# Kernel optimization log

Measured on AMD Instinct MI355X. Metric: run time of the kernel, lower is better.

## Reference

```python
import jax, jax.numpy as jnp
import numpy as np

B, C_IN, H, W = 4, 2048, 64, 64
C_INTER = C_IN // 4          # 512
C_QK = C_INTER // 8          # 64
C_OUT = 512


def conv3x3(x, w):
    # x: [B,C,H,W], w: [O,I,3,3], padding=1, no bias
    return jax.lax.conv_general_dilated(
        x, w, window_strides=(1, 1), padding=((1, 1), (1, 1)),
        dimension_numbers=('NCHW', 'OIHW', 'NCHW'))


def criss_cross_attention(x, qw, kw, vw, gamma):
    # x: [B,Ci,H,W]; qw,kw: [Cqk,Ci]; vw: [Ci,Ci]; gamma: scalar
    b, c, h, w = x.shape
    q = jnp.einsum('bchw,oc->bohw', x, qw)
    k = jnp.einsum('bchw,oc->bohw', x, kw)
    v = jnp.einsum('bchw,oc->bohw', x, vw)
    # column (H-axis) affinity with -inf diagonal to avoid double self-count
    eH = jnp.einsum('bchw,bciw->bhwi', q, k)                  # [B,H,W,H]
    diag = jnp.eye(h, dtype=bool)[None, :, None, :]           # [1,H,1,H]
    eH = jnp.where(diag, -jnp.inf, eH)
    # row (W-axis) affinity
    eW = jnp.einsum('bchw,bchj->bhwj', q, k)                  # [B,H,W,W]
    att = jax.nn.softmax(jnp.concatenate([eH, eW], axis=-1), axis=-1)
    attH, attW = att[..., :h], att[..., h:]
    outH = jnp.einsum('bhwi,bciw->bchw', attH, v)
    outW = jnp.einsum('bhwj,bchj->bchw', attW, v)
    return gamma * (outH + outW) + x


def setup_inputs() -> dict:
    key = jax.random.key(0)
    ks = jax.random.split(key, 8)
    s = 0.02
    return {
        'x': jax.random.normal(ks[0], (B, C_IN, H, W), jnp.float32),
        'conva_w': jax.random.normal(ks[1], (C_INTER, C_IN, 3, 3), jnp.float32) * s,
        'q_w': jax.random.normal(ks[2], (C_QK, C_INTER), jnp.float32) * s,
        'k_w': jax.random.normal(ks[3], (C_QK, C_INTER), jnp.float32) * s,
        'v_w': jax.random.normal(ks[4], (C_INTER, C_INTER), jnp.float32) * s,
        'gamma': jax.random.normal(ks[5], (), jnp.float32) * 0.1,
        'convb_w': jax.random.normal(ks[6], (C_INTER, C_INTER, 3, 3), jnp.float32) * s,
        'bottleneck_w': jax.random.normal(ks[7], (C_OUT, C_IN + C_INTER, 3, 3), jnp.float32) * s,
        'recurrence': 2,
    }


def reference(x, conva_w, q_w, k_w, v_w, gamma, convb_w, bottleneck_w, recurrence):
    out = conv3x3(x, conva_w)
    for _ in range(recurrence):
        out = criss_cross_attention(out, q_w, k_w, v_w, gamma)
    out = conv3x3(out, convb_w)
    out = conv3x3(jnp.concatenate([x, out], axis=1), bottleneck_w)
    return out
```

## Files before the change

### kernel.cpp

```cpp
#include <hip/hip_runtime.h>
#include <hip/hip_bf16.h>
#include <stdint.h>

typedef unsigned short u16;
typedef __bf16 bf16x8 __attribute__((ext_vector_type(8)));
typedef float f32x4 __attribute__((ext_vector_type(4)));

#define DEVINL __device__ __forceinline__

DEVINL float bf2f(u16 v) {
    union { uint32_t u; float f; } c; c.u = ((uint32_t)v) << 16; return c.f;
}
DEVINL u16 f2bf(float f) {
    union { float f; uint32_t u; } c; c.f = f;
    uint32_t x = c.u;
    x += 0x7fffu + ((x >> 16) & 1u);
    return (u16)(x >> 16);
}

DEVINL void load_lds16(const u16* g, char* lds_uniform_base) {
    __builtin_amdgcn_global_load_lds(
        (const __attribute__((address_space(1))) void*)g,
        (__attribute__((address_space(3))) void*)lds_uniform_base,
        16, 0, 0);
}

template<int OM>
__launch_bounds__(256)
__global__ void conv_gemm(const u16* __restrict__ in, int IH, int IW, int inC, int cofs,
                          int K, int ntaps, const u16* __restrict__ wt, int N,
                          void* __restrict__ outp, int outC, int nwg)
{
    __shared__ __align__(16) u16 ldsA[2][8192];
    __shared__ __align__(16) u16 ldsB[2][8192];

    const int id  = blockIdx.x;
    const int swz = (id & 7) * (nwg >> 3) + (id >> 3);
    const int m0 = (swz & 127) << 7;
    const int n0 = (swz >> 7) << 7;

    const int tid  = threadIdx.x;
    const int lane = tid & 63;
    const int wv   = tid >> 6;
    const int l7 = lane & 7, l3 = lane >> 3;
    const int g  = lane >> 4;
    const int cOff = (l7 ^ l3) << 3;

    const int wn = (wv & 1) * 64;
    const int wm = (wv >> 1) * 64;

    f32x4 acc[4][4];
#pragma unroll
    for (int i = 0; i < 4; ++i)
#pragma unroll
        for (int j = 0; j < 4; ++j) acc[i][j] = (f32x4){0.f, 0.f, 0.f, 0.f};

    const u16* aBase = wt + (size_t)(n0 + wv * 32 + l3) * K + cOff;
    const u16* bBase[4];
#pragma unroll
    for (int q = 0; q < 4; ++q) {
        int mA = m0 + wv * 32 + q * 8 + l3;
        int bb = mA >> 12, yy = (mA >> 6) & 63, xx = mA & 63;
        bBase[q] = in + ((size_t)(bb * IH + yy) * IW + xx) * inC + cofs + cOff;
    }

    const int kpt = K >> 6;
    const int nsteps = ntaps * kpt;
    int s_tap = 0, s_k0 = 0;
    size_t s_wofs = 0;
    int s_xofs = 0;

    auto STAGE = [&](int buf) {
        char* la = (char*)ldsA[buf] + wv * 4096;
        char* lb = (char*)ldsB[buf] + wv * 4096;
        const u16* wp = aBase + s_wofs;
        const int xo = s_xofs;
#pragma unroll
        for (int q = 0; q < 4; ++q) {
            load_lds16(wp + (size_t)(q * 8) * K, la + q * 1024);
            load_lds16(bBase[q] + xo,            lb + q * 1024);
        }
    };
    auto ADV = [&]() {
        ++s_tap;
        if (s_tap == ntaps) { s_tap = 0; s_k0 += 64; }
        int ty = s_tap / 3, tx = s_tap % 3;
        s_wofs = (size_t)s_tap * N * K + s_k0;
        s_xofs = (ty * IW + tx) * inC + s_k0;
    };

    STAGE(0); ADV();
    int cur = 0;
    const int rb = (lane & 15) << 7;

    for (int s = 0; s < nsteps; ++s) {
        __syncthreads();
        if (s + 1 < nsteps) { STAGE(cur ^ 1); ADV(); }

        const char* laW = (const char*)ldsA[cur] + (wn << 7);
        const char* lbW = (const char*)ldsB[cur] + (wm << 7);
#pragma unroll
        for (int kk = 0; kk < 2; ++kk) {
            const int ca = (((kk << 2) + g) ^ l7) << 4;
            bf16x8 af[4], bfr[4];
#pragma unroll
            for (int f = 0; f < 4; ++f) {
                af[f]  = *(const bf16x8*)(laW + (f << 11) + rb + ca);
                bfr[f] = *(const bf16x8*)(lbW + (f << 11) + rb + ca);
            }
#pragma unroll
            for (int fn = 0; fn < 4; ++fn)
#pragma unroll
                for (int fm = 0; fm < 4; ++fm)
                    acc[fn][fm] = __builtin_amdgcn_mfma_f32_16x16x32_bf16(
                        af[fn], bfr[fm], acc[fn][fm], 0, 0, 0);
        }
        cur ^= 1;
    }

    const int rn = (lane >> 4) * 4;
    const int cm = lane & 15;
#pragma unroll
    for (int fn = 0; fn < 4; ++fn) {
#pragma unroll
        for (int fm = 0; fm < 4; ++fm) {
            const int n = n0 + wn + fn * 16 + rn;
            const int m = m0 + wm + fm * 16 + cm;
            const int b = m >> 12, y = (m >> 6) & 63, x = m & 63;
            f32x4 v = acc[fn][fm];
            if constexpr (OM == 1) {
                ushort4 pk;
                pk.x = f2bf(v[0]); pk.y = f2bf(v[1]); pk.z = f2bf(v[2]); pk.w = f2bf(v[3]);
                *(ushort4*)((u16*)outp + (size_t)m * outC + n) = pk;
            } else if constexpr (OM == 2) {
                ushort4 pk;
                pk.x = f2bf(v[0]); pk.y = f2bf(v[1]); pk.z = f2bf(v[2]); pk.w = f2bf(v[3]);
                size_t o = ((size_t)(b * 66 + y + 1) * 66 + (x + 1)) * 2560 + 2048 + n;
                *(ushort4*)((u16*)outp + o) = pk;
            } else {
                float* op = (float*)outp;
#pragma unroll
                for (int r = 0; r < 4; ++r)
                    op[((size_t)(b * 512 + n + r) << 12) + (y << 6) + x] = v[r];
            }
        }
    }
}


__global__ void wtrans(const float* __restrict__ w, u16* __restrict__ wo, int O, int C)
{
    int idx = blockIdx.x * 256 + threadIdx.x;
    int total = O * C;
    if (idx >= total) return;
    const float* src = w + (size_t)idx * 9;
    float v[9];
#pragma unroll
    for (int t = 0; t < 9; ++t) v[t] = src[t];
#pragma unroll
    for (int t = 0; t < 9; ++t) wo[(size_t)t * total + idx] = f2bf(v[t]);
}

__global__ void wqkv_concat(const float* __restrict__ q, const float* __restrict__ k,
                            const float* __restrict__ v, u16* __restrict__ o)
{
    int idx = blockIdx.x * 256 + threadIdx.x;
    if (idx >= 640 * 512) return;
    int row = idx >> 9;
    float val = (row < 64) ? q[idx] : (row < 128) ? k[idx - 64 * 512] : v[idx - 128 * 512];
    o[idx] = f2bf(val);
}

__global__ void nchw_to_nhwc_pad(const float* __restrict__ x, u16* __restrict__ xp)
{
    size_t idx = (size_t)blockIdx.x * 256 + threadIdx.x;
    int m  = (int)(idx & 16383);
    int cc = (int)(idx >> 14);
    int xw = m & 63, y = (m >> 6) & 63, b = m >> 12;
    const float* xs = x + ((size_t)(b * 2048 + cc * 8)) * 4096 + (y << 6) + xw;
    union { u16 u[8]; uint4 v4; } tmp;
#pragma unroll
    for (int j = 0; j < 8; ++j) tmp.u[j] = f2bf(xs[(size_t)j * 4096]);
    u16* dst = xp + ((size_t)(b * 66 + y + 1) * 66 + (xw + 1)) * 2560 + cc * 8;
    *(uint4*)dst = tmp.v4;
}

__global__ void pad512(const u16* __restrict__ F, u16* __restrict__ FP)
{
    size_t idx = (size_t)blockIdx.x * 256 + threadIdx.x;
    int cc = (int)(idx & 63);
    int m  = (int)(idx >> 6);
    int xw = m & 63, y = (m >> 6) & 63, b = m >> 12;
    const uint4* src = (const uint4*)(F + (size_t)m * 512 + cc * 8);
    uint4* dst = (uint4*)(FP + ((size_t)(b * 66 + y + 1) * 66 + (xw + 1)) * 512 + cc * 8);
    *dst = *src;
}

__global__ void zero_border(u16* __restrict__ P, int C)
{
    int idx = blockIdx.x * 256 + threadIdx.x;
    int cw = C >> 3;
    int total = 4 * 260 * cw;
    if (idx >= total) return;
    int ch   = (idx % cw) * 8;
    int cell = (idx / cw) % 260;
    int b    = idx / (cw * 260);
    int y, x;
    if (cell < 66)       { y = 0;              x = cell;       }
    else if (cell < 132) { y = 65;             x = cell - 66;  }
    else if (cell < 196) { y = cell - 132 + 1; x = 0;          }
    else                 { y = cell - 196 + 1; x = 65;         }
    size_t o = ((size_t)(b * 66 + y) * 66 + x) * C + ch;
    *(uint4*)(P + o) = (uint4){0, 0, 0, 0};
}

__global__ void fill7777(float* __restrict__ o, int n)
{
    int idx = blockIdx.x * 256 + threadIdx.x;
    if (idx < n) o[idx] = 7777.0f;
}

#define NEGBIG -1.0e30f

__global__ void att_score(const u16* __restrict__ QKV, float* __restrict__ ATT)
{
    const int bid0 = blockIdx.x;
    const bool isW = bid0 >= 512;
    const int bid = bid0 & 511;
    const int half = bid >> 8;
    const int b = (bid >> 6) & 3, rc = bid & 63;
    __shared__ float q[32][65], kk[64][65];
    const int tid = threadIdx.x;
    for (int p = tid; p < 2048; p += 256) {
        int r = p >> 6, c = p & 63;
        int row = half * 32 + r;
        size_t m = isW ? (size_t)((b << 12) + (rc << 6) + row)
                       : (size_t)((b << 12) + (row << 6) + rc);
        q[r][c] = bf2f(QKV[m * 640 + c]);
    }
    for (int p = tid; p < 4096; p += 256) {
        int r = p >> 6, c = p & 63;
        size_t m = isW ? (size_t)((b << 12) + (rc << 6) + r)
                       : (size_t)((b << 12) + (r << 6) + rc);
        kk[r][c] = bf2f(QKV[m * 640 + 64 + c]);
    }
    __syncthreads();
    for (int p = tid; p < 2048; p += 256) {
        int r = p >> 6, i = p & 63;
        float s = 0.f;
#pragma unroll 8
        for (int c = 0; c < 64; ++c) s += q[r][c] * kk[i][c];
        int row = half * 32 + r;
        if (!isW) {
            if (i == row) s = NEGBIG;
            ATT[(size_t)((b << 12) + (row << 6) + rc) * 128 + i] = s;
        } else {
            ATT[(size_t)((b << 12) + (rc << 6) + row) * 128 + 64 + i] = s;
        }
    }
}

DEVINL void softmax32(float (*A)[132], int tid)
{
    const int row = tid >> 3, sub = tid & 7;
    float lm = -3.4e38f;
#pragma unroll
    for (int i = sub * 16; i < sub * 16 + 16; ++i) lm = fmaxf(lm, A[row][i]);
    lm = fmaxf(lm, __shfl_xor(lm, 1));
    lm = fmaxf(lm, __shfl_xor(lm, 2));
    lm = fmaxf(lm, __shfl_xor(lm, 4));
    float ls = 0.f;
#pragma unroll
    for (int i = sub * 16; i < sub * 16 + 16; ++i) {
        float e = __expf(A[row][i] - lm);
        A[row][i] = e;
        ls += e;
    }
    ls += __shfl_xor(ls, 1);
    ls += __shfl_xor(ls, 2);
    ls += __shfl_xor(ls, 4);
    float inv = 1.f / ls;
#pragma unroll
    for (int i = sub * 16; i < sub * 16 + 16; ++i) A[row][i] *= inv;
}

__launch_bounds__(256)
__global__ void att_outH(const u16* __restrict__ QKV, const float* __restrict__ ATT,
                         float* __restrict__ OH)
{
    const int bid = blockIdx.x;
    const int half = bid >> 8;
    const int b = (bid >> 6) & 3, x = bid & 63;
    __shared__ float A[32][132];
    const int tid = threadIdx.x;
    for (int p = tid; p < 1024; p += 256) {
        int r = p >> 5, q4 = p & 31;
        *(f32x4*)&A[r][q4 * 4] = *(const f32x4*)
            &ATT[(size_t)((b << 12) + ((half * 32 + r) << 6) + x) * 128 + q4 * 4];
    }
    __syncthreads();
    softmax32(A, tid);
    __syncthreads();
    const int wv = tid >> 6, lane = tid & 63;
    const int r0 = wv * 8;
    float acc[8][8];
#pragma unroll
    for (int cc = 0; cc < 8; ++cc)
#pragma unroll
        for (int yy = 0; yy < 8; ++yy) acc[cc][yy] = 0.f;
    for (int i = 0; i < 64; ++i) {
        float a[8];
#pragma unroll
        for (int yy = 0; yy < 8; ++yy) a[yy] = A[r0 + yy][i];
        const u16* vrow = QKV + (size_t)((b << 12) + (i << 6) + x) * 640 + 128;
#pragma unroll
        for (int cc = 0; cc < 8; ++cc) {
            float v = bf2f(vrow[cc * 64 + lane]);
#pragma unroll
            for (int yy = 0; yy < 8; ++yy) acc[cc][yy] += a[yy] * v;
        }
    }
    const int y0 = half * 32 + r0;
#pragma unroll
    for (int cc = 0; cc < 8; ++cc)
#pragma unroll
        for (int yy = 0; yy < 8; ++yy)
            OH[(size_t)((b << 12) + ((y0 + yy) << 6) + x) * 512 + cc * 64 + lane]
                = acc[cc][yy];
}

__launch_bounds__(256)
__global__ void att_outW_combine(const u16* __restrict__ QKV, const float* __restrict__ ATT,
                                 const float* __restrict__ OH, const u16* __restrict__ Fin,
                                 u16* __restrict__ Fout, const float* __restrict__ gamma)
{
    const int bid = blockIdx.x;
    const int half = bid >> 8;
    const int b = (bid >> 6) & 3, y = bid & 63;
    const size_t mb = (size_t)((b << 12) + (y << 6));
    __shared__ float A[32][132];
    const int tid = threadIdx.x;
    for (int p = tid; p < 1024; p += 256) {
        int r = p >> 5, q4 = p & 31;
        *(f32x4*)&A[r][q4 * 4] = *(const f32x4*)
            &ATT[(mb + half * 32 + r) * 128 + q4 * 4];
    }
    const float g = gamma[0];
    __syncthreads();
    softmax32(A, tid);
    __syncthreads();
    const int wv = tid >> 6, lane = tid & 63;
    const int r0 = wv * 8;
    float acc[8][8];
#pragma unroll
    for (int cc = 0; cc < 8; ++cc)
#pragma unroll
        for (int xx = 0; xx < 8; ++xx) acc[cc][xx] = 0.f;
    for (int j = 0; j < 64; ++j) {
        float a[8];
#pragma unroll
        for (int xx = 0; xx < 8; ++xx) a[xx] = A[r0 + xx][64 + j];
        const u16* vrow = QKV + (mb + j) * 640 + 128;
#pragma unroll
        for (int cc = 0; cc < 8; ++cc) {
            float v = bf2f(vrow[cc * 64 + lane]);
#pragma unroll
            for (int xx = 0; xx < 8; ++xx) acc[cc][xx] += a[xx] * v;
        }
    }
    const int x0 = half * 32 + r0;
#pragma unroll
    for (int cc = 0; cc < 8; ++cc) {
#pragma unroll
        for (int xx = 0; xx < 8; ++xx) {
            size_t m = mb + x0 + xx;
            size_t o = m * 512 + cc * 64 + lane;
            Fout[o] = f2bf(g * (OH[o] + acc[cc][xx]) + bf2f(Fin[o]));
        }
    }
}

static constexpr size_t ALN = 512;
static inline size_t alup(size_t v) { return (v + ALN - 1) & ~(ALN - 1); }

extern "C" void kernel_launch(void* const* d_in, const int* in_sizes, int n_in,
                              void* d_out, int out_size, void* d_ws, size_t ws_size,
                              hipStream_t stream)
{
    (void)in_sizes; (void)n_in;
    const float* x       = (const float*)d_in[0];
    const float* conva_w = (const float*)d_in[1];
    const float* q_w     = (const float*)d_in[2];
    const float* k_w     = (const float*)d_in[3];
    const float* v_w     = (const float*)d_in[4];
    const float* gamma   = (const float*)d_in[5];
    const float* convb_w = (const float*)d_in[6];
    const float* bneck_w = (const float*)d_in[7];

    const size_t XP_B   = (size_t)4 * 66 * 66 * 2560 * 2;
    const size_t WB_B   = (size_t)9 * 512 * 512 * 2;
    const size_t WQKV_B = (size_t)640 * 512 * 2;
    const size_t F_B    = (size_t)4 * 4096 * 512 * 2;
    const size_t QKV_B  = (size_t)4 * 4096 * 640 * 2;
    const size_t ATT_B  = (size_t)4 * 4096 * 128 * 4;
    const size_t WA_B   = (size_t)9 * 512 * 2048 * 2;
    const size_t FP_B   = (size_t)4 * 66 * 66 * 512 * 2;
    const size_t WN_B   = (size_t)9 * 512 * 2560 * 2;

    size_t arena_B = alup(QKV_B) + alup(ATT_B);
    if (alup(FP_B) + alup(WN_B) > arena_B) arena_B = alup(FP_B) + alup(WN_B);
    if (alup(WA_B) > arena_B) arena_B = alup(WA_B);

    const size_t NEED = alup(XP_B) + alup(WB_B) + alup(WQKV_B) + 2 * alup(F_B) + arena_B;
    if (ws_size < NEED) {
        fill7777<<<(out_size + 255) / 256, 256, 0, stream>>>((float*)d_out, out_size);
        return;
    }

    char* p = (char*)d_ws;
    u16* XP   = (u16*)p; p += alup(XP_B);
    u16* WB   = (u16*)p; p += alup(WB_B);
    u16* WQKV = (u16*)p; p += alup(WQKV_B);
    u16* F0   = (u16*)p; p += alup(F_B);
    u16* F1   = (u16*)p; p += alup(F_B);
    char* arena = p;
    u16*   WA  = (u16*)arena;
    u16*   QKV = (u16*)arena;
    float* ATT = (float*)(arena + alup(QKV_B));
    u16*   FP  = (u16*)arena;
    u16*   WN  = (u16*)(arena + alup(FP_B));
    float* OH  = (float*)d_out;

    zero_border<<<(4 * 260 * (2560 / 8) + 255) / 256, 256, 0, stream>>>(XP, 2560);

    wtrans<<<(512 * 2048 + 255) / 256, 256, 0, stream>>>(conva_w, WA, 512, 2048);
    wtrans<<<(512 * 512 + 255) / 256, 256, 0, stream>>>(convb_w, WB, 512, 512);
    wqkv_concat<<<(640 * 512 + 255) / 256, 256, 0, stream>>>(q_w, k_w, v_w, WQKV);

    nchw_to_nhwc_pad<<<16384, 256, 0, stream>>>(x, XP);

    conv_gemm<1><<<512, 256, 0, stream>>>(XP, 66, 66, 2560, 0, 2048, 9,
                                          WA, 512, F0, 512, 512);

    const u16* Fi = F0;
    u16* Fo = F1;
    for (int it = 0; it < 2; ++it) {
        conv_gemm<1><<<640, 256, 0, stream>>>(Fi, 64, 64, 512, 0, 512, 1,
                                              WQKV, 640, QKV, 640, 640);
        att_score<<<1024, 256, 0, stream>>>(QKV, ATT);
        att_outH<<<512, 256, 0, stream>>>(QKV, ATT, OH);
        att_outW_combine<<<512, 256, 0, stream>>>(QKV, ATT, OH, Fi, Fo, gamma);
        const u16* t = Fi; Fi = Fo; Fo = (u16*)t;
    }

    zero_border<<<(4 * 260 * (512 / 8) + 255) / 256, 256, 0, stream>>>(FP, 512);
    pad512<<<4096, 256, 0, stream>>>(Fi, FP);
    wtrans<<<(512 * 2560 + 255) / 256, 256, 0, stream>>>(bneck_w, WN, 512, 2560);

    conv_gemm<2><<<512, 256, 0, stream>>>(FP, 66, 66, 512, 0, 512, 9,
                                          WB, 512, XP, 2560, 512);

    conv_gemm<3><<<512, 256, 0, stream>>>(XP, 66, 66, 2560, 0, 2560, 9,
                                          WN, 512, d_out, 512, 512);
}
```

Measured before the change: 1.103 ms.

## Split-K the two large 3x3 conv GEMMs across twice as many workgroups

Adds a conv_gemm32 kernel that splits the reduction dimension in half, so the first conv and the bottleneck conv launch 1024 workgroups instead of 512. Each half-K partial goes to its own buffer, and a separate elementwise kernel then adds the two partials: bf16 for the first conv, f32 into the output for the bottleneck. The new kernel also stages 32-wide K chunks per step with double-buffered LDS. The aim is more workgroups per CU for better latency hiding and load balance, at the cost of extra partial-write and reduction traffic, one more launch per conv, and some precision loss from rounding the bf16 partials.

Measured after the change: 1.361 ms. 1.23x slower.

```diff
diff --git a/kernel.cpp b/kernel.cpp
--- a/kernel.cpp
+++ b/kernel.cpp
@@ -147,6 +147,151 @@
     }
 }
 
+template<int OM>
+__launch_bounds__(256)
+__global__ void conv_gemm32(const u16* __restrict__ in, int IH, int IW, int inC, int cofs,
+                            int K, int ntaps, const u16* __restrict__ wt, int N,
+                            void* __restrict__ outp0, void* __restrict__ outp1,
+                            int outC, int nwg)
+{
+    __shared__ __align__(16) u16 ldsA[2][4096];
+    __shared__ __align__(16) u16 ldsB[2][4096];
+
+    const int id  = blockIdx.x;
+    const int swz = (id & 7) * (nwg >> 3) + (id >> 3);
+    const int kspl = swz & 1;
+    const int tile = swz >> 1;
+    const int m0 = (tile & 127) << 7;
+    const int n0 = (tile >> 7) << 7;
+    const int k_lo = kspl * (K >> 1);
+    void* outp = kspl ? outp1 : outp0;
+
+    const int tid  = threadIdx.x;
+    const int lane = tid & 63;
+    const int wv   = tid >> 6;
+    const int g    = lane >> 4;
+    const int r4   = lane >> 2;
+    const int hs   = (r4 + (r4 >> 2)) & 3;
+    const int cOff = (((lane & 3) ^ hs) << 3);
+
+    const int wn = (wv & 1) * 64;
+    const int wm = (wv >> 1) * 64;
+
+    f32x4 acc[4][4];
+#pragma unroll
+    for (int i = 0; i < 4; ++i)
+#pragma unroll
+        for (int j = 0; j < 4; ++j) acc[i][j] = (f32x4){0.f, 0.f, 0.f, 0.f};
+
+    const u16* aB[2];
+#pragma unroll
+    for (int j = 0; j < 2; ++j)
+        aB[j] = wt + (size_t)(n0 + wv * 32 + j * 16 + r4) * K + cOff;
+    const u16* bB[2];
+#pragma unroll
+    for (int j = 0; j < 2; ++j) {
+        int mA = m0 + wv * 32 + j * 16 + r4;
+        int bb = mA >> 12, yy = (mA >> 6) & 63, xx = mA & 63;
+        bB[j] = in + ((size_t)(bb * IH + yy) * IW + xx) * inC + cofs + cOff;
+    }
+
+    const int nsteps = ntaps * (K >> 6);
+    int s_tap = 0, s_k0 = k_lo;
+    size_t s_wofs = k_lo;
+    int s_xofs = k_lo;
+
+    auto STAGE = [&](int buf) {
+        char* la = (char*)ldsA[buf] + wv * 2048;
+        char* lb = (char*)ldsB[buf] + wv * 2048;
+        const u16* w0 = aB[0] + s_wofs;
+        const u16* w1 = aB[1] + s_wofs;
+        const int xo = s_xofs;
+        load_lds16(w0,          la);
+        load_lds16(w1,          la + 1024);
+        load_lds16(bB[0] + xo,  lb);
+        load_lds16(bB[1] + xo,  lb + 1024);
+    };
+    auto ADV = [&]() {
+        ++s_tap;
+        if (s_tap == ntaps) { s_tap = 0; s_k0 += 32; }
+        int ty = s_tap / 3, tx = s_tap % 3;
+        s_wofs = (size_t)s_tap * N * K + s_k0;
+        s_xofs = (ty * IW + tx) * inC + s_k0;
+    };
+
+    STAGE(0); ADV();
+    int cur = 0;
+    const int R  = lane & 15;
+    const int hR = (R + (R >> 2)) & 3;
+    const int rsOff = (R << 6) + ((g ^ hR) << 4);
+
+    for (int s = 0; s < nsteps; ++s) {
+        __syncthreads();
+        if (s + 1 < nsteps) { STAGE(cur ^ 1); ADV(); }
+
+        const char* laW = (const char*)ldsA[cur] + (wn << 6) + rsOff;
+        const char* lbW = (const char*)ldsB[cur] + (wm << 6) + rsOff;
+        bf16x8 af[4], bfr[4];
+#pragma unroll
+        for (int f = 0; f < 4; ++f) {
+            af[f]  = *(const bf16x8*)(laW + (f << 10));
+            bfr[f] = *(const bf16x8*)(lbW + (f << 10));
+        }
+#pragma unroll
+        for (int fn = 0; fn < 4; ++fn)
+#pragma unroll
+            for (int fm = 0; fm < 4; ++fm)
+                acc[fn][fm] = __builtin_amdgcn_mfma_f32_16x16x32_bf16(
+                    af[fn], bfr[fm], acc[fn][fm], 0, 0, 0);
+        cur ^= 1;
+    }
+
+    const int rn = (lane >> 4) * 4;
+    const int cm = lane & 15;
+#pragma unroll
+    for (int fn = 0; fn < 4; ++fn) {
+#pragma unroll
+        for (int fm = 0; fm < 4; ++fm) {
+            const int n = n0 + wn + fn * 16 + rn;
+            const int m = m0 + wm + fm * 16 + cm;
+            const int b = m >> 12, y = (m >> 6) & 63, x = m & 63;
+            f32x4 v = acc[fn][fm];
+            if constexpr (OM == 1) {
+                ushort4 pk;
+                pk.x = f2bf(v[0]); pk.y = f2bf(v[1]); pk.z = f2bf(v[2]); pk.w = f2bf(v[3]);
+                *(ushort4*)((u16*)outp + (size_t)m * outC + n) = pk;
+            } else {
+                float* op = (float*)outp;
+#pragma unroll
+                for (int r = 0; r < 4; ++r)
+                    op[((size_t)(b * 512 + n + r) << 12) + (y << 6) + x] = v[r];
+            }
+        }
+    }
+}
+
+__global__ void addf32(float* __restrict__ dst, const float* __restrict__ src, int n4)
+{
+    int i = blockIdx.x * 256 + threadIdx.x;
+    if (i >= n4) return;
+    f32x4 a = ((const f32x4*)src)[i];
+    f32x4 d = ((f32x4*)dst)[i];
+    ((f32x4*)dst)[i] = (f32x4){d[0] + a[0], d[1] + a[1], d[2] + a[2], d[3] + a[3]};
+}
+
+__global__ void addbf16(u16* __restrict__ dst, const u16* __restrict__ a,
+                        const u16* __restrict__ b, int n8)
+{
+    int i = blockIdx.x * 256 + threadIdx.x;
+    if (i >= n8) return;
+    union { u16 u[8]; uint4 v; } va, vb, vo;
+    va.v = ((const uint4*)a)[i];
+    vb.v = ((const uint4*)b)[i];
+#pragma unroll
+    for (int j = 0; j < 8; ++j) vo.u[j] = f2bf(bf2f(va.u[j]) + bf2f(vb.u[j]));
+    ((uint4*)dst)[i] = vo.v;
+}
+
 
 __global__ void wtrans(const float* __restrict__ w, u16* __restrict__ wo, int O, int C)
 {
@@ -409,7 +554,7 @@
 
     size_t arena_B = alup(QKV_B) + alup(ATT_B);
     if (alup(FP_B) + alup(WN_B) > arena_B) arena_B = alup(FP_B) + alup(WN_B);
-    if (alup(WA_B) > arena_B) arena_B = alup(WA_B);
+    if (alup(WA_B) + alup(F_B) > arena_B) arena_B = alup(WA_B) + alup(F_B);
 
     const size_t NEED = alup(XP_B) + alup(WB_B) + alup(WQKV_B) + 2 * alup(F_B) + arena_B;
     if (ws_size < NEED) {
@@ -425,11 +570,13 @@
     u16* F1   = (u16*)p; p += alup(F_B);
     char* arena = p;
     u16*   WA  = (u16*)arena;
+    u16*   PA  = (u16*)(arena + alup(WA_B));
     u16*   QKV = (u16*)arena;
     float* ATT = (float*)(arena + alup(QKV_B));
     u16*   FP  = (u16*)arena;
     u16*   WN  = (u16*)(arena + alup(FP_B));
     float* OH  = (float*)d_out;
+    float* FHALF = (float*)F0;
 
     zero_border<<<(4 * 260 * (2560 / 8) + 255) / 256, 256, 0, stream>>>(XP, 2560);
 
@@ -439,8 +586,9 @@
 
     nchw_to_nhwc_pad<<<16384, 256, 0, stream>>>(x, XP);
 
-    conv_gemm<1><<<512, 256, 0, stream>>>(XP, 66, 66, 2560, 0, 2048, 9,
-                                          WA, 512, F0, 512, 512);
+    conv_gemm32<1><<<1024, 256, 0, stream>>>(XP, 66, 66, 2560, 0, 2048, 9,
+                                             WA, 512, F1, PA, 512, 1024);
+    addbf16<<<(1048576 + 255) / 256, 256, 0, stream>>>(F0, F1, PA, 1048576);
 
     const u16* Fi = F0;
     u16* Fo = F1;
@@ -460,6 +608,7 @@
     conv_gemm<2><<<512, 256, 0, stream>>>(FP, 66, 66, 512, 0, 512, 9,
                                           WB, 512, XP, 2560, 512);
 
-    conv_gemm<3><<<512, 256, 0, stream>>>(XP, 66, 66, 2560, 0, 2560, 9,
-                                          WN, 512, d_out, 512, 512);
-}
+    conv_gemm32<3><<<1024, 256, 0, stream>>>(XP, 66, 66, 2560, 0, 2560, 9,
+                                             WN, 512, FHALF, d_out, 512, 1024);
+    addf32<<<(2097152 + 255) / 256, 256, 0, stream>>>((float*)d_out, FHALF, 2097152);
+}
```
